# Optimization experiments

Hardware: AMD Instinct MI355X
Metric: run time of the kernel (lower is better)

## Reference

```python
import jax, jax.numpy as jnp
import numpy as np

N_NODES = 100000


def sage_conv(x, edge_index, Wl, Wr, b):
    # PyG SAGEConv(aggr='mean'): out = lin_l(mean_{j in N(i)} x_j) + lin_r(x_i)
    src, dst = edge_index[0], edge_index[1]
    msg = x[src]                                    # [E, d] gather
    agg = jax.ops.segment_sum(msg, dst, num_segments=N_NODES)
    cnt = jax.ops.segment_sum(jnp.ones((src.shape[0],), dtype=x.dtype), dst,
                              num_segments=N_NODES)
    mean = agg / jnp.maximum(cnt, 1.0)[:, None]     # isolated nodes -> 0
    return mean @ Wl + x @ Wr + b


def setup_inputs() -> dict:
    key = jax.random.key(0)
    ks = jax.random.split(key, 7)
    N, E, d_in, d_hid, d_out = N_NODES, 1000000, 64, 128, 64
    x = jax.random.normal(ks[0], (N, d_in), dtype=jnp.float32)
    W1l = jax.random.normal(ks[1], (d_in, d_hid), dtype=jnp.float32) / np.sqrt(d_in)
    W1r = jax.random.normal(ks[2], (d_in, d_hid), dtype=jnp.float32) / np.sqrt(d_in)
    b1 = jnp.zeros((d_hid,), dtype=jnp.float32)
    W2l = jax.random.normal(ks[3], (d_hid, d_out), dtype=jnp.float32) / np.sqrt(d_hid)
    W2r = jax.random.normal(ks[4], (d_hid, d_out), dtype=jnp.float32) / np.sqrt(d_hid)
    b2 = jnp.zeros((d_out,), dtype=jnp.float32)
    edge_index = jax.random.randint(ks[5], (2, E), 0, N, dtype=jnp.int64)
    return {"x": x, "W1l": W1l, "W1r": W1r, "b1": b1,
            "W2l": W2l, "W2r": W2r, "b2": b2, "edge_index": edge_index}


def reference(x, W1l, W1r, b1, W2l, W2r, b2, edge_index):
    h = jax.nn.relu(sage_conv(x, edge_index, W1l, W1r, b1))
    out = sage_conv(h, edge_index, W2l, W2r, b2)
    return out
```

## Files before the change

### kernel.cpp

```cpp
#include <hip/hip_runtime.h>

#define N_NODES 100000
#define N_EDGES 1000000
#define DEG_CAP 64
#define OVF_CAP 4096
#define SPILL_CAP 4096

#define BKT_SH 8
#define BKT_NODES 256
#define NBKT 392
#define BKT_CAP 4096
#define BIN_CHUNK 4096
#define FIFO_CAP 32

typedef __attribute__((ext_vector_type(8))) short bf16x8;
typedef __attribute__((ext_vector_type(4))) float f32x4;

__device__ __forceinline__ unsigned short f2bf(float f) {
    unsigned u = __float_as_uint(f);
    return (unsigned short)((u + 0x7FFF + ((u >> 16) & 1)) >> 16);
}
__device__ __forceinline__ float bf2f(unsigned short b) {
    return __uint_as_float(((unsigned)b) << 16);
}
__device__ __forceinline__ float bflo(unsigned u) {
    return __uint_as_float(u << 16);
}
__device__ __forceinline__ float bfhi(unsigned u) {
    return __uint_as_float(u & 0xffff0000u);
}
__device__ __forceinline__ void split_rbf(float f, unsigned short& ho,
                                          unsigned short& lo) {
    unsigned short hb = f2bf(f);
    ho = hb;
    lo = f2bf(f - bf2f(hb));
}


__global__ __launch_bounds__(256) void prep_kernel(
        const float4* __restrict__ x4,
        ushort4* __restrict__ xh4, ushort4* __restrict__ xl4,
        const float* __restrict__ W1l, const float* __restrict__ W1r,
        const float* __restrict__ W2l, const float* __restrict__ W2r,
        short* __restrict__ Bf1, short* __restrict__ Bf2,
        int4* __restrict__ gcur4, int* __restrict__ ovfc,
        int* __restrict__ spillc) {
    int i = blockIdx.x * blockDim.x + threadIdx.x;
    if (i < 128) gcur4[i] = make_int4(0, 0, 0, 0);
    if (i == 0) { *ovfc = 0; *spillc = 0; }
    if (i < 32768) {
        int g = i >> 14;
        int e = i & 16383;
        int k = e >> 7;
        int n = e & 127;
        float v;
        if (g == 0) v = (k < 64) ? W1l[k * 128 + n] : W1r[(k - 64) * 128 + n];
        else        v = (n < 64) ? W2l[k * 64 + n]  : W2r[k * 64 + (n - 64)];
        unsigned short hb, lb;
        split_rbf(v, hb, lb);
        int c = n >> 4, kc = k >> 5;
        int lane = (((k >> 3) & 3) << 4) | (n & 15);
        int j = k & 7;
        short* base = g ? Bf2 : Bf1;
        base[((c * 4 + kc) * 2 + 0) * 512 + lane * 8 + j] = (short)hb;
        base[((c * 4 + kc) * 2 + 1) * 512 + lane * 8 + j] = (short)lb;
    }
    if (i < N_NODES * 16) {
        float4 v = x4[i];
        ushort4 oh, ol;
        split_rbf(v.x, oh.x, ol.x);
        split_rbf(v.y, oh.y, ol.y);
        split_rbf(v.z, oh.z, ol.z);
        split_rbf(v.w, oh.w, ol.w);
        xh4[i] = oh;
        xl4[i] = ol;
    }
}

__global__ __launch_bounds__(256) void bin_kernel(
        const int* __restrict__ ei, unsigned* __restrict__ rec,
        int* __restrict__ gcur, int* __restrict__ spillc,
        int2* __restrict__ spill) {
    __shared__ int lcnt[NBKT];
    __shared__ unsigned fifo[NBKT * FIFO_CAP];
    for (int i = threadIdx.x; i < NBKT; i += 256) lcnt[i] = 0;
    __syncthreads();
    int base = blockIdx.x * BIN_CHUNK;
    int end = base + BIN_CHUNK;
    if (end > N_EDGES) end = N_EDGES;
    for (int e = base + threadIdx.x; e < end; e += 256) {
        int s = ei[e];
        int d = ei[N_EDGES + e];
        int b = d >> BKT_SH;
        unsigned r = ((unsigned)s << BKT_SH) | (unsigned)(d & (BKT_NODES - 1));
        int pos = atomicAdd(&lcnt[b], 1);
        if (pos < FIFO_CAP) {
            fifo[b * FIFO_CAP + pos] = r;
        } else {
            int o = atomicAdd(spillc, 1);
            if (o < SPILL_CAP) spill[o] = make_int2(s, d);
        }
    }
    __syncthreads();
    for (int b = threadIdx.x; b < NBKT; b += 256) {
        int cnt = lcnt[b];
        if (cnt > FIFO_CAP) cnt = FIFO_CAP;
        if (cnt == 0) continue;
        int gb = atomicAdd(&gcur[b], cnt);
        for (int k = 0; k < cnt; ++k) {
            int g = gb + k;
            unsigned r = fifo[b * FIFO_CAP + k];
            if (g < BKT_CAP) {
                rec[b * BKT_CAP + g] = r;
            } else {
                int o = atomicAdd(spillc, 1);
                if (o < SPILL_CAP)
                    spill[o] = make_int2((int)(r >> BKT_SH),
                                         (b << BKT_SH) | (int)(r & (BKT_NODES - 1)));
            }
        }
    }
}

__global__ __launch_bounds__(256) void build_kernel(
        const unsigned* __restrict__ rec, const int* __restrict__ gcur,
        const int2* __restrict__ spill, const int* __restrict__ spillc,
        int* __restrict__ counts, int* __restrict__ slots,
        int* __restrict__ ovfc, int* __restrict__ ovf) {
    __shared__ int lcnt[BKT_NODES];
    __shared__ int lslots[BKT_NODES * DEG_CAP];
    int b = blockIdx.x;
    for (int i = threadIdx.x; i < BKT_NODES; i += 256) lcnt[i] = 0;
    __syncthreads();
    int n = gcur[b];
    if (n > BKT_CAP) n = BKT_CAP;
    for (int i = threadIdx.x; i < n; i += 256) {
        unsigned r = rec[b * BKT_CAP + i];
        int dlo = (int)(r & (BKT_NODES - 1));
        int src = (int)(r >> BKT_SH);
        int pos = atomicAdd(&lcnt[dlo], 1);
        if (pos < DEG_CAP) {
            lslots[dlo * DEG_CAP + pos] = src;
        } else {
            int o = atomicAdd(ovfc, 1);
            if (o < OVF_CAP) {
                ovf[o * 2] = src;
                ovf[o * 2 + 1] = (b << BKT_SH) | dlo;
            }
        }
    }
    int ns = *spillc;
    if (ns > SPILL_CAP) ns = SPILL_CAP;
    for (int i = threadIdx.x; i < ns; i += 256) {
        int2 e = spill[i];
        if ((e.y >> BKT_SH) == b) {
            int dlo = e.y & (BKT_NODES - 1);
            int pos = atomicAdd(&lcnt[dlo], 1);
            if (pos < DEG_CAP) {
                lslots[dlo * DEG_CAP + pos] = e.x;
            } else {
                int o = atomicAdd(ovfc, 1);
                if (o < OVF_CAP) { ovf[o * 2] = e.x; ovf[o * 2 + 1] = e.y; }
            }
        }
    }
    __syncthreads();
    int nodeBase = b << BKT_SH;
    for (int i = threadIdx.x; i < BKT_NODES; i += 256)
        counts[nodeBase + i] = lcnt[i];
    const int4* ls4 = (const int4*)lslots;
    int4* gs4 = (int4*)(slots + nodeBase * DEG_CAP);
    for (int i = threadIdx.x; i < BKT_NODES * DEG_CAP / 4; i += 256)
        gs4[i] = ls4[i];
}

__global__ __launch_bounds__(256) void gather_bf_kernel(
        const unsigned short* __restrict__ feat, const int* __restrict__ counts,
        const int* __restrict__ slots,
        unsigned short* __restrict__ mh, unsigned short* __restrict__ ml) {
    int wid = blockIdx.x * 4 + (threadIdx.x >> 6);
    int l = threadIdx.x & 63;
    if (wid >= N_NODES) return;
    int deg = counts[wid];
    int dcap = min(deg, DEG_CAP);
    int ids = slots[wid * DEG_CAP + l];
    const int grp = l >> 4;
    const int fb = (l & 15) * 4;
    float s0 = 0.f, s1 = 0.f, s2 = 0.f, s3 = 0.f;
    int j = 0;
    for (; j + 8 <= dcap; j += 8) {
        int sA = __shfl(ids, j + grp);
        int sB = __shfl(ids, j + 4 + grp);
        uint2 uA = *(const uint2*)(feat + sA * 64 + fb);
        uint2 uB = *(const uint2*)(feat + sB * 64 + fb);
        s0 += bflo(uA.x) + bflo(uB.x);
        s1 += bfhi(uA.x) + bfhi(uB.x);
        s2 += bflo(uA.y) + bflo(uB.y);
        s3 += bfhi(uA.y) + bfhi(uB.y);
    }
    for (; j < dcap; j += 4) {
        int nb = j + grp;
        bool v = nb < dcap;
        int s = __shfl(ids, v ? nb : 0);
        uint2 u = *(const uint2*)(feat + s * 64 + fb);
        if (v) {
            s0 += bflo(u.x);
            s1 += bfhi(u.x);
            s2 += bflo(u.y);
            s3 += bfhi(u.y);
        }
    }
    s0 += __shfl_xor(s0, 16); s0 += __shfl_xor(s0, 32);
    s1 += __shfl_xor(s1, 16); s1 += __shfl_xor(s1, 32);
    s2 += __shfl_xor(s2, 16); s2 += __shfl_xor(s2, 32);
    s3 += __shfl_xor(s3, 16); s3 += __shfl_xor(s3, 32);
    if (l < 16) {
        float inv = 1.0f / fmaxf((float)deg, 1.0f);
        ushort4 oh, ol;
        split_rbf(s0 * inv, oh.x, ol.x);
        split_rbf(s1 * inv, oh.y, ol.y);
        split_rbf(s2 * inv, oh.z, ol.z);
        split_rbf(s3 * inv, oh.w, ol.w);
        *(ushort4*)&mh[wid * 64 + fb] = oh;
        *(ushort4*)&ml[wid * 64 + fb] = ol;
    }
}

__global__ __launch_bounds__(256) void mlp_fused_kernel(
        const unsigned short* __restrict__ mh, const unsigned short* __restrict__ ml,
        const unsigned short* __restrict__ xh, const unsigned short* __restrict__ xl,
        const float* __restrict__ x,
        const short* __restrict__ Bf1, const float* __restrict__ b1,
        const short* __restrict__ Bf2, const float* __restrict__ b2,
        const int* __restrict__ ovf, const int* __restrict__ ovfc,
        const int* __restrict__ counts,
        unsigned short* __restrict__ p_bf_out, float* __restrict__ q) {
    __shared__ unsigned short h_lds[128][136];
    const int w = threadIdx.x >> 6;
    const int l = threadIdx.x & 63;
    const int lane15 = l & 15;
    const int quad = l >> 4;
    const int rowBase = blockIdx.x * 128;

    {
        int n = *ovfc;
        if (n > OVF_CAP) n = OVF_CAP;
        if (n > 0) {
            for (int idx = 0; idx < n; ++idx) {
                int d = ovf[idx * 2 + 1];
                if (d >= rowBase && d < rowBase + 128) {
                    if (threadIdx.x < 64) {
                        int s = ovf[idx * 2];
                        int t = threadIdx.x;
                        float inv = 1.0f / fmaxf((float)counts[d], 1.0f);
                        float m = bf2f(mh[d * 64 + t]) + bf2f(ml[d * 64 + t])
                                + x[s * 64 + t] * inv;
                        unsigned short hb, lb;
                        split_rbf(m, hb, lb);
                        ((unsigned short*)mh)[d * 64 + t] = hb;
                        ((unsigned short*)ml)[d * 64 + t] = lb;
                    }
                    __syncthreads();
                }
            }
            __syncthreads();
        }
    }

    {
        bf16x8 bh[2][4], bl[2][4];
#pragma unroll
        for (int ci = 0; ci < 2; ++ci) {
            const int c = 2 * w + ci;
#pragma unroll
            for (int kc = 0; kc < 4; ++kc) {
                const short* bp = Bf1 + ((c * 4 + kc) * 2) * 512 + l * 8;
                bh[ci][kc] = *(const bf16x8*)bp;
                bl[ci][kc] = *(const bf16x8*)(bp + 512);
            }
        }
        float bias[2];
#pragma unroll
        for (int ci = 0; ci < 2; ++ci) bias[ci] = b1[(2 * w + ci) * 16 + lane15];

#pragma unroll
        for (int rt = 0; rt < 8; ++rt) {
            const int row = rowBase + rt * 16 + lane15;
            const bool rv = row < N_NODES;
            const bf16x8 zz = {0, 0, 0, 0, 0, 0, 0, 0};

            bf16x8 ah[4], al[4];
#pragma unroll
            for (int kc = 0; kc < 4; ++kc) {
                if (rv) {
                    const int off = (kc < 2)
                        ? row * 64 + kc * 32 + quad * 8
                        : row * 64 + (kc - 2) * 32 + quad * 8;
                    const unsigned short* ph = (kc < 2) ? (mh + off) : (xh + off);
                    const unsigned short* pl = (kc < 2) ? (ml + off) : (xl + off);
                    ah[kc] = *(const bf16x8*)ph;
                    al[kc] = *(const bf16x8*)pl;
                } else {
                    ah[kc] = zz;
                    al[kc] = zz;
                }
            }

            f32x4 acc[2] = {(f32x4){0.f, 0.f, 0.f, 0.f}, (f32x4){0.f, 0.f, 0.f, 0.f}};
#pragma unroll
            for (int kc = 0; kc < 4; ++kc) {
#pragma unroll
                for (int ci = 0; ci < 2; ++ci) {
                    acc[ci] = __builtin_amdgcn_mfma_f32_16x16x32_bf16(ah[kc], bh[ci][kc], acc[ci], 0, 0, 0);
                    acc[ci] = __builtin_amdgcn_mfma_f32_16x16x32_bf16(al[kc], bh[ci][kc], acc[ci], 0, 0, 0);
                    acc[ci] = __builtin_amdgcn_mfma_f32_16x16x32_bf16(ah[kc], bl[ci][kc], acc[ci], 0, 0, 0);
                }
            }

            const int rloc = rt * 16 + quad * 4;
#pragma unroll
            for (int ci = 0; ci < 2; ++ci) {
                const int col = (2 * w + ci) * 16 + lane15;
#pragma unroll
                for (int i = 0; i < 4; ++i)
                    h_lds[rloc + i][col] =
                        f2bf(fmaxf(acc[ci][i] + bias[ci], 0.f));
            }
        }
    }
    __syncthreads();

    {
        bf16x8 bh[2][4], bl[2][4];
#pragma unroll
        for (int ci = 0; ci < 2; ++ci) {
            const int c = 2 * w + ci;
#pragma unroll
            for (int kc = 0; kc < 4; ++kc) {
                const short* bp = Bf2 + ((c * 4 + kc) * 2) * 512 + l * 8;
                bh[ci][kc] = *(const bf16x8*)bp;
                bl[ci][kc] = *(const bf16x8*)(bp + 512);
            }
        }
        float bias[2];
#pragma unroll
        for (int ci = 0; ci < 2; ++ci) {
            const int c = 2 * w + ci;
            bias[ci] = (c >= 4) ? b2[(c - 4) * 16 + lane15] : 0.f;
        }

#pragma unroll
        for (int rt = 0; rt < 8; ++rt) {
            bf16x8 ah[4];
#pragma unroll
            for (int kc = 0; kc < 4; ++kc)
                ah[kc] = *(const bf16x8*)&h_lds[rt * 16 + lane15][kc * 32 + quad * 8];

            f32x4 acc[2] = {(f32x4){0.f, 0.f, 0.f, 0.f}, (f32x4){0.f, 0.f, 0.f, 0.f}};
#pragma unroll
            for (int kc = 0; kc < 4; ++kc) {
#pragma unroll
                for (int ci = 0; ci < 2; ++ci) {
                    acc[ci] = __builtin_amdgcn_mfma_f32_16x16x32_bf16(ah[kc], bh[ci][kc], acc[ci], 0, 0, 0);
                    acc[ci] = __builtin_amdgcn_mfma_f32_16x16x32_bf16(ah[kc], bl[ci][kc], acc[ci], 0, 0, 0);
                }
            }

            const int rb = rowBase + rt * 16 + quad * 4;
#pragma unroll
            for (int ci = 0; ci < 2; ++ci) {
                const int c = 2 * w + ci;
                if (c < 4) {
#pragma unroll
                    for (int i = 0; i < 4; ++i) {
                        int r = rb + i;
                        if (r < N_NODES)
                            p_bf_out[r * 64 + c * 16 + lane15] = f2bf(acc[ci][i]);
                    }
                } else {
#pragma unroll
                    for (int i = 0; i < 4; ++i) {
                        int r = rb + i;
                        if (r < N_NODES)
                            q[r * 64 + (c - 4) * 16 + lane15] = acc[ci][i] + bias[ci];
                    }
                }
            }
        }
    }
}

__global__ __launch_bounds__(256) void gather_final_kernel(
        const unsigned short* __restrict__ p, const int* __restrict__ counts,
        const int* __restrict__ slots, const float* __restrict__ q,
        const int* __restrict__ ovf, const int* __restrict__ ovfc,
        float* __restrict__ out) {
    int wid = blockIdx.x * 4 + (threadIdx.x >> 6);
    int l = threadIdx.x & 63;
    if (wid >= N_NODES) return;
    int deg = counts[wid];
    int dcap = min(deg, DEG_CAP);
    int ids = slots[wid * DEG_CAP + l];
    const int grp = l >> 4;
    const int fb = (l & 15) * 4;
    float s0 = 0.f, s1 = 0.f, s2 = 0.f, s3 = 0.f;
    int j = 0;
    for (; j + 8 <= dcap; j += 8) {
        int sA = __shfl(ids, j + grp);
        int sB = __shfl(ids, j + 4 + grp);
        uint2 uA = *(const uint2*)(p + sA * 64 + fb);
        uint2 uB = *(const uint2*)(p + sB * 64 + fb);
        s0 += bflo(uA.x) + bflo(uB.x);
        s1 += bfhi(uA.x) + bfhi(uB.x);
        s2 += bflo(uA.y) + bflo(uB.y);
        s3 += bfhi(uA.y) + bfhi(uB.y);
    }
    for (; j < dcap; j += 4) {
        int nb = j + grp;
        bool v = nb < dcap;
        int s = __shfl(ids, v ? nb : 0);
        uint2 u = *(const uint2*)(p + s * 64 + fb);
        if (v) {
            s0 += bflo(u.x);
            s1 += bfhi(u.x);
            s2 += bflo(u.y);
            s3 += bfhi(u.y);
        }
    }
    s0 += __shfl_xor(s0, 16); s0 += __shfl_xor(s0, 32);
    s1 += __shfl_xor(s1, 16); s1 += __shfl_xor(s1, 32);
    s2 += __shfl_xor(s2, 16); s2 += __shfl_xor(s2, 32);
    s3 += __shfl_xor(s3, 16); s3 += __shfl_xor(s3, 32);
    if (l < 16) {
        int n = *ovfc;
        if (n > OVF_CAP) n = OVF_CAP;
        for (int idx = 0; idx < n; ++idx) {
            if (ovf[idx * 2 + 1] == wid) {
                int s = ovf[idx * 2];
                uint2 u = *(const uint2*)(p + s * 64 + fb);
                s0 += bflo(u.x);
                s1 += bfhi(u.x);
                s2 += bflo(u.y);
                s3 += bfhi(u.y);
            }
        }
        float inv = 1.0f / fmaxf((float)deg, 1.0f);
        float4 qv = *(const float4*)&q[wid * 64 + fb];
        *(float4*)&out[wid * 64 + fb] =
            make_float4(s0 * inv + qv.x, s1 * inv + qv.y,
                        s2 * inv + qv.z, s3 * inv + qv.w);
    }
}

extern "C" void kernel_launch(void* const* d_in, const int* in_sizes, int n_in,
                              void* d_out, int out_size, void* d_ws, size_t ws_size,
                              hipStream_t stream) {
    const float* x   = (const float*)d_in[0];
    const float* W1l = (const float*)d_in[1];
    const float* W1r = (const float*)d_in[2];
    const float* b1  = (const float*)d_in[3];
    const float* W2l = (const float*)d_in[4];
    const float* W2r = (const float*)d_in[5];
    const float* b2  = (const float*)d_in[6];
    const int*   ei  = (const int*)d_in[7];

    int*   wsi      = (int*)d_ws;
    float* wsf      = (float*)d_ws;
    int*   counts   = wsi;
    int*   ovfc     = wsi + 100352;
    int*   spillc   = wsi + 100353;
    int*   gcur     = wsi + 100416;
    int*   ovf      = wsi + 100928;
    int2*  spill    = (int2*)(wsi + 109120);
    short* Bf1      = (short*)(wsi + 117312);
    short* Bf2      = (short*)(wsi + 133696);
    int*   slots    = wsi + 150080;
    unsigned* rec   = (unsigned*)(wsi + 6572608);
    unsigned short* xh = (unsigned short*)(wsi + 8178240);
    unsigned short* xl = (unsigned short*)(wsi + 11378240);
    unsigned short* mh = (unsigned short*)(wsi + 14578240);
    unsigned short* ml = (unsigned short*)(wsi + 17778240);
    unsigned short* p_bf = (unsigned short*)(wsi + 20978240);
    float* q        = wsf + 24178240;
    float* out      = (float*)d_out;

    prep_kernel<<<(N_NODES * 16 + 255) / 256, 256, 0, stream>>>(
        (const float4*)x, (ushort4*)xh, (ushort4*)xl, W1l, W1r, W2l, W2r,
        Bf1, Bf2, (int4*)gcur, ovfc, spillc);

    bin_kernel<<<(N_EDGES + BIN_CHUNK - 1) / BIN_CHUNK, 256, 0, stream>>>(
        ei, rec, gcur, spillc, spill);
    build_kernel<<<NBKT, 256, 0, stream>>>(
        rec, gcur, spill, spillc, counts, slots, ovfc, ovf);

    gather_bf_kernel<<<(N_NODES + 3) / 4, 256, 0, stream>>>(
        xh, counts, slots, mh, ml);

    mlp_fused_kernel<<<(N_NODES + 127) / 128, 256, 0, stream>>>(
        mh, ml, xh, xl, x, Bf1, b1, Bf2, b2, ovf, ovfc, counts, p_bf, q);

    gather_final_kernel<<<(N_NODES + 3) / 4, 256, 0, stream>>>(
        p_bf, counts, slots, q, ovf, ovfc, out);
}
```

Measured before the change: 228.5 us.

## Map each node to 16 lanes in gather kernels instead of a full wave

Both neighbour-gather kernels now assign a 16-lane group per node (16 nodes per block) rather than a 64-lane wavefront. Each lane handles 4 features and walks the neighbour list serially, fetching slot indices in 16-entry phases and broadcasting them with shuffles. This removes the cross-lane xor reductions and the idle lanes in the epilogue. In exchange it serialises neighbour loads per node and exposes the wave to degree divergence among its four nodes.

```diff
diff --git a/kernel.cpp b/kernel.cpp
--- a/kernel.cpp
+++ b/kernel.cpp
@@ -178,52 +178,48 @@
         const unsigned short* __restrict__ feat, const int* __restrict__ counts,
         const int* __restrict__ slots,
         unsigned short* __restrict__ mh, unsigned short* __restrict__ ml) {
-    int wid = blockIdx.x * 4 + (threadIdx.x >> 6);
-    int l = threadIdx.x & 63;
-    if (wid >= N_NODES) return;
-    int deg = counts[wid];
+    int node = blockIdx.x * 16 + (threadIdx.x >> 4);
+    int t = threadIdx.x & 15;
+    if (node >= N_NODES) return;
+    int deg = counts[node];
     int dcap = min(deg, DEG_CAP);
-    int ids = slots[wid * DEG_CAP + l];
-    const int grp = l >> 4;
-    const int fb = (l & 15) * 4;
-    float s0 = 0.f, s1 = 0.f, s2 = 0.f, s3 = 0.f;
-    int j = 0;
-    for (; j + 8 <= dcap; j += 8) {
-        int sA = __shfl(ids, j + grp);
-        int sB = __shfl(ids, j + 4 + grp);
-        uint2 uA = *(const uint2*)(feat + sA * 64 + fb);
-        uint2 uB = *(const uint2*)(feat + sB * 64 + fb);
-        s0 += bflo(uA.x) + bflo(uB.x);
-        s1 += bfhi(uA.x) + bfhi(uB.x);
-        s2 += bflo(uA.y) + bflo(uB.y);
-        s3 += bfhi(uA.y) + bfhi(uB.y);
-    }
-    for (; j < dcap; j += 4) {
-        int nb = j + grp;
-        bool v = nb < dcap;
-        int s = __shfl(ids, v ? nb : 0);
-        uint2 u = *(const uint2*)(feat + s * 64 + fb);
-        if (v) {
-            s0 += bflo(u.x);
-            s1 += bfhi(u.x);
-            s2 += bflo(u.y);
-            s3 += bfhi(u.y);
-        }
-    }
-    s0 += __shfl_xor(s0, 16); s0 += __shfl_xor(s0, 32);
-    s1 += __shfl_xor(s1, 16); s1 += __shfl_xor(s1, 32);
-    s2 += __shfl_xor(s2, 16); s2 += __shfl_xor(s2, 32);
-    s3 += __shfl_xor(s3, 16); s3 += __shfl_xor(s3, 32);
-    if (l < 16) {
-        float inv = 1.0f / fmaxf((float)deg, 1.0f);
-        ushort4 oh, ol;
-        split_rbf(s0 * inv, oh.x, ol.x);
-        split_rbf(s1 * inv, oh.y, ol.y);
-        split_rbf(s2 * inv, oh.z, ol.z);
-        split_rbf(s3 * inv, oh.w, ol.w);
-        *(ushort4*)&mh[wid * 64 + fb] = oh;
-        *(ushort4*)&ml[wid * 64 + fb] = ol;
-    }
+    const int gbase = threadIdx.x & 48;
+    float a0 = 0.f, a1 = 0.f, a2 = 0.f, a3 = 0.f;
+    for (int phase = 0; phase * 16 < dcap; ++phase) {
+        int ids16 = slots[node * DEG_CAP + phase * 16 + t];
+        int lim = min(dcap - phase * 16, 16);
+        int j = 0;
+        for (; j + 4 <= lim; j += 4) {
+            int s0 = __shfl(ids16, gbase | (j + 0));
+            int s1 = __shfl(ids16, gbase | (j + 1));
+            int s2 = __shfl(ids16, gbase | (j + 2));
+            int s3 = __shfl(ids16, gbase | (j + 3));
+            uint2 u0 = *(const uint2*)(feat + s0 * 64 + t * 4);
+            uint2 u1 = *(const uint2*)(feat + s1 * 64 + t * 4);
+            uint2 u2 = *(const uint2*)(feat + s2 * 64 + t * 4);
+            uint2 u3 = *(const uint2*)(feat + s3 * 64 + t * 4);
+            a0 += bflo(u0.x) + bflo(u1.x) + bflo(u2.x) + bflo(u3.x);
+            a1 += bfhi(u0.x) + bfhi(u1.x) + bfhi(u2.x) + bfhi(u3.x);
+            a2 += bflo(u0.y) + bflo(u1.y) + bflo(u2.y) + bflo(u3.y);
+            a3 += bfhi(u0.y) + bfhi(u1.y) + bfhi(u2.y) + bfhi(u3.y);
+        }
+        for (; j < lim; ++j) {
+            int s = __shfl(ids16, gbase | j);
+            uint2 u = *(const uint2*)(feat + s * 64 + t * 4);
+            a0 += bflo(u.x);
+            a1 += bfhi(u.x);
+            a2 += bflo(u.y);
+            a3 += bfhi(u.y);
+        }
+    }
+    float inv = 1.0f / fmaxf((float)deg, 1.0f);
+    ushort4 oh, ol;
+    split_rbf(a0 * inv, oh.x, ol.x);
+    split_rbf(a1 * inv, oh.y, ol.y);
+    split_rbf(a2 * inv, oh.z, ol.z);
+    split_rbf(a3 * inv, oh.w, ol.w);
+    *(ushort4*)&mh[node * 64 + t * 4] = oh;
+    *(ushort4*)&ml[node * 64 + t * 4] = ol;
 }
 
 __global__ __launch_bounds__(256) void mlp_fused_kernel(
@@ -395,61 +391,57 @@
         const int* __restrict__ slots, const float* __restrict__ q,
         const int* __restrict__ ovf, const int* __restrict__ ovfc,
         float* __restrict__ out) {
-    int wid = blockIdx.x * 4 + (threadIdx.x >> 6);
-    int l = threadIdx.x & 63;
-    if (wid >= N_NODES) return;
-    int deg = counts[wid];
+    int node = blockIdx.x * 16 + (threadIdx.x >> 4);
+    int t = threadIdx.x & 15;
+    if (node >= N_NODES) return;
+    int deg = counts[node];
     int dcap = min(deg, DEG_CAP);
-    int ids = slots[wid * DEG_CAP + l];
-    const int grp = l >> 4;
-    const int fb = (l & 15) * 4;
-    float s0 = 0.f, s1 = 0.f, s2 = 0.f, s3 = 0.f;
-    int j = 0;
-    for (; j + 8 <= dcap; j += 8) {
-        int sA = __shfl(ids, j + grp);
-        int sB = __shfl(ids, j + 4 + grp);
-        uint2 uA = *(const uint2*)(p + sA * 64 + fb);
-        uint2 uB = *(const uint2*)(p + sB * 64 + fb);
-        s0 += bflo(uA.x) + bflo(uB.x);
-        s1 += bfhi(uA.x) + bfhi(uB.x);
-        s2 += bflo(uA.y) + bflo(uB.y);
-        s3 += bfhi(uA.y) + bfhi(uB.y);
-    }
-    for (; j < dcap; j += 4) {
-        int nb = j + grp;
-        bool v = nb < dcap;
-        int s = __shfl(ids, v ? nb : 0);
-        uint2 u = *(const uint2*)(p + s * 64 + fb);
-        if (v) {
-            s0 += bflo(u.x);
-            s1 += bfhi(u.x);
-            s2 += bflo(u.y);
-            s3 += bfhi(u.y);
-        }
-    }
-    s0 += __shfl_xor(s0, 16); s0 += __shfl_xor(s0, 32);
-    s1 += __shfl_xor(s1, 16); s1 += __shfl_xor(s1, 32);
-    s2 += __shfl_xor(s2, 16); s2 += __shfl_xor(s2, 32);
-    s3 += __shfl_xor(s3, 16); s3 += __shfl_xor(s3, 32);
-    if (l < 16) {
-        int n = *ovfc;
-        if (n > OVF_CAP) n = OVF_CAP;
-        for (int idx = 0; idx < n; ++idx) {
-            if (ovf[idx * 2 + 1] == wid) {
-                int s = ovf[idx * 2];
-                uint2 u = *(const uint2*)(p + s * 64 + fb);
-                s0 += bflo(u.x);
-                s1 += bfhi(u.x);
-                s2 += bflo(u.y);
-                s3 += bfhi(u.y);
-            }
-        }
-        float inv = 1.0f / fmaxf((float)deg, 1.0f);
-        float4 qv = *(const float4*)&q[wid * 64 + fb];
-        *(float4*)&out[wid * 64 + fb] =
-            make_float4(s0 * inv + qv.x, s1 * inv + qv.y,
-                        s2 * inv + qv.z, s3 * inv + qv.w);
-    }
+    const int gbase = threadIdx.x & 48;
+    float a0 = 0.f, a1 = 0.f, a2 = 0.f, a3 = 0.f;
+    for (int phase = 0; phase * 16 < dcap; ++phase) {
+        int ids16 = slots[node * DEG_CAP + phase * 16 + t];
+        int lim = min(dcap - phase * 16, 16);
+        int j = 0;
+        for (; j + 4 <= lim; j += 4) {
+            int s0 = __shfl(ids16, gbase | (j + 0));
+            int s1 = __shfl(ids16, gbase | (j + 1));
+            int s2 = __shfl(ids16, gbase | (j + 2));
+            int s3 = __shfl(ids16, gbase | (j + 3));
+            uint2 u0 = *(const uint2*)(p + s0 * 64 + t * 4);
+            uint2 u1 = *(const uint2*)(p + s1 * 64 + t * 4);
+            uint2 u2 = *(const uint2*)(p + s2 * 64 + t * 4);
+            uint2 u3 = *(const uint2*)(p + s3 * 64 + t * 4);
+            a0 += bflo(u0.x) + bflo(u1.x) + bflo(u2.x) + bflo(u3.x);
+            a1 += bfhi(u0.x) + bfhi(u1.x) + bfhi(u2.x) + bfhi(u3.x);
+            a2 += bflo(u0.y) + bflo(u1.y) + bflo(u2.y) + bflo(u3.y);
+            a3 += bfhi(u0.y) + bfhi(u1.y) + bfhi(u2.y) + bfhi(u3.y);
+        }
+        for (; j < lim; ++j) {
+            int s = __shfl(ids16, gbase | j);
+            uint2 u = *(const uint2*)(p + s * 64 + t * 4);
+            a0 += bflo(u.x);
+            a1 += bfhi(u.x);
+            a2 += bflo(u.y);
+            a3 += bfhi(u.y);
+        }
+    }
+    int n = *ovfc;
+    if (n > OVF_CAP) n = OVF_CAP;
+    for (int idx = 0; idx < n; ++idx) {
+        if (ovf[idx * 2 + 1] == node) {
+            int s = ovf[idx * 2];
+            uint2 u = *(const uint2*)(p + s * 64 + t * 4);
+            a0 += bflo(u.x);
+            a1 += bfhi(u.x);
+            a2 += bflo(u.y);
+            a3 += bfhi(u.y);
+        }
+    }
+    float inv = 1.0f / fmaxf((float)deg, 1.0f);
+    float4 qv = *(const float4*)&q[node * 64 + t * 4];
+    *(float4*)&out[node * 64 + t * 4] =
+        make_float4(a0 * inv + qv.x, a1 * inv + qv.y,
+                    a2 * inv + qv.z, a3 * inv + qv.w);
 }
 
 extern "C" void kernel_launch(void* const* d_in, const int* in_sizes, int n_in,
@@ -493,12 +485,12 @@
     build_kernel<<<NBKT, 256, 0, stream>>>(
         rec, gcur, spill, spillc, counts, slots, ovfc, ovf);
 
-    gather_bf_kernel<<<(N_NODES + 3) / 4, 256, 0, stream>>>(
+    gather_bf_kernel<<<(N_NODES + 15) / 16, 256, 0, stream>>>(
         xh, counts, slots, mh, ml);
 
     mlp_fused_kernel<<<(N_NODES + 127) / 128, 256, 0, stream>>>(
         mh, ml, xh, xl, x, Bf1, b1, Bf2, b2, ovf, ovfc, counts, p_bf, q);
 
-    gather_final_kernel<<<(N_NODES + 3) / 4, 256, 0, stream>>>(
+    gather_final_kernel<<<(N_NODES + 15) / 16, 256, 0, stream>>>(
         p_bf, counts, slots, q, ovf, ovfc, out);
 }
```

Measured after the change: 215.2 us. 1.06x faster.
